# Performance work log

Measured on AMD Instinct MI355X. Metric: run time of the kernel, lower is better.

## Reference

```python
import jax, jax.numpy as jnp
import numpy as np


def setup_inputs() -> dict:
    key = jax.random.key(0)
    k1, k2 = jax.random.split(key)
    B, N, M, D = 4, 4096, 4096, 32
    x1 = jax.random.normal(k1, (B, N, D), dtype=jnp.float32)
    x2 = jax.random.normal(k2, (B, M, D), dtype=jnp.float32)
    const = jnp.ones((1,), dtype=jnp.float32)
    return {"x1": x1, "x2": x2, "const": const}


def reference(x1, x2, const):
    # Pairwise dot products: [B,N,D] x [B,M,D] -> [B,N,M], then add scalar bias.
    # (Original materializes an O(N*M*D) broadcast intermediate; einsum/bmm avoids it.)
    numerator = jnp.einsum("bnd,bmd->bnm", x1, x2)
    return numerator + const
```

## Files before the change

kernel.cpp:

```cpp
#include <hip/hip_runtime.h>


constexpr int Bv = 4;
constexpr int Nv = 4096;
constexpr int Mv = 4096;
constexpr int Dv = 32;
constexpr int TM = 128;
constexpr int TN = 256;
constexpr int LRA = 132;
constexpr int LRB = 260;

__global__ __launch_bounds__(256, 2)
void pairwise_dot_bias_kernel(const float* __restrict__ x1,
                              const float* __restrict__ x2,
                              const float* __restrict__ cbias,
                              float* __restrict__ out) {
    __shared__ float a_s[Dv][LRA];
    __shared__ float b_s[Dv][LRB];

    const int b  = blockIdx.z;
    const int n0 = blockIdx.y * TM;
    const int m0 = blockIdx.x * TN;
    const int t  = threadIdx.x;

    const float* x1b = x1 + (size_t)b * Nv * Dv + (size_t)n0 * Dv;
    const float* x2b = x2 + (size_t)b * Mv * Dv + (size_t)m0 * Dv;

    #pragma unroll
    for (int p = 0; p < 4; ++p) {
        const int flat = p * 1024 + t * 4;
        const int row  = flat >> 5;
        const int col  = flat & 31;
        const float4 av = *reinterpret_cast<const float4*>(x1b + flat);
        a_s[col + 0][row] = av.x;
        a_s[col + 1][row] = av.y;
        a_s[col + 2][row] = av.z;
        a_s[col + 3][row] = av.w;
    }
    #pragma unroll
    for (int p = 0; p < 8; ++p) {
        const int flat = p * 1024 + t * 4;
        const int row  = flat >> 5;
        const int col  = flat & 31;
        const float4 bv = *reinterpret_cast<const float4*>(x2b + flat);
        b_s[col + 0][row] = bv.x;
        b_s[col + 1][row] = bv.y;
        b_s[col + 2][row] = bv.z;
        b_s[col + 3][row] = bv.w;
    }
    __syncthreads();

    const int tx = t & 15;
    const int ty = t >> 4;

    float acc[8][16];
    #pragma unroll
    for (int i = 0; i < 8; ++i)
        #pragma unroll
        for (int j = 0; j < 16; ++j)
            acc[i][j] = 0.0f;

    #pragma unroll 2
    for (int d = 0; d < Dv; ++d) {
        const float4 a0 = *reinterpret_cast<const float4*>(&a_s[d][ty * 8]);
        const float4 a1 = *reinterpret_cast<const float4*>(&a_s[d][ty * 8 + 4]);
        const float4 b0 = *reinterpret_cast<const float4*>(&b_s[d][tx * 4]);
        const float4 b1 = *reinterpret_cast<const float4*>(&b_s[d][64 + tx * 4]);
        const float4 b2 = *reinterpret_cast<const float4*>(&b_s[d][128 + tx * 4]);
        const float4 b3 = *reinterpret_cast<const float4*>(&b_s[d][192 + tx * 4]);
        const float av[8]  = {a0.x, a0.y, a0.z, a0.w, a1.x, a1.y, a1.z, a1.w};
        const float bw[16] = {b0.x, b0.y, b0.z, b0.w, b1.x, b1.y, b1.z, b1.w,
                              b2.x, b2.y, b2.z, b2.w, b3.x, b3.y, b3.z, b3.w};
        #pragma unroll
        for (int i = 0; i < 8; ++i)
            #pragma unroll
            for (int j = 0; j < 16; ++j)
                acc[i][j] = fmaf(av[i], bw[j], acc[i][j]);
    }

    const float cb = cbias[0];
    float* outb = out + (size_t)b * Nv * Mv;
    #pragma unroll
    for (int i = 0; i < 8; ++i) {
        float* orow = outb + (size_t)(n0 + ty * 8 + i) * Mv + m0;
        #pragma unroll
        for (int h = 0; h < 4; ++h) {
            float4 v;
            v.x = acc[i][h * 4 + 0] + cb;
            v.y = acc[i][h * 4 + 1] + cb;
            v.z = acc[i][h * 4 + 2] + cb;
            v.w = acc[i][h * 4 + 3] + cb;
            *reinterpret_cast<float4*>(orow + h * 64 + tx * 4) = v;
        }
    }
}

extern "C" void kernel_launch(void* const* d_in, const int* in_sizes, int n_in,
                              void* d_out, int out_size, void* d_ws, size_t ws_size,
                              hipStream_t stream) {
    const float* x1 = (const float*)d_in[0];
    const float* x2 = (const float*)d_in[1];
    const float* cb = (const float*)d_in[2];
    float* out = (float*)d_out;

    dim3 grid(Mv / TN, Nv / TM, Bv);
    pairwise_dot_bias_kernel<<<grid, 256, 0, stream>>>(x1, x2, cb, out);
}
```

Before: 66.75 us.

## Loop each block over four N-tiles with double-buffered A prefetch and nontemporal stores

Each block now keeps its x2 tile resident in LDS and walks four consecutive 128-row x1 tiles. It prefetches the next x1 tile into registers while the current tile computes, and writes it into a second LDS buffer after the output stores. Output writes switch to nontemporal stores so they do not pollute the cache. This cuts the grid size and redundant B loads and overlaps global loads with compute, at the cost of more LDS, more registers for the prefetch, and less block-level parallelism.

```diff
diff --git a/kernel.cpp b/kernel.cpp
--- a/kernel.cpp
+++ b/kernel.cpp
@@ -1,5 +1,7 @@
 #include <hip/hip_runtime.h>
 
+
+typedef float v4f __attribute__((ext_vector_type(4)));
 
 constexpr int Bv = 4;
 constexpr int Nv = 4096;
@@ -7,6 +9,7 @@
 constexpr int Dv = 32;
 constexpr int TM = 128;
 constexpr int TN = 256;
+constexpr int NT = 4;
 constexpr int LRA = 132;
 constexpr int LRB = 260;
 
@@ -15,82 +18,114 @@
                               const float* __restrict__ x2,
                               const float* __restrict__ cbias,
                               float* __restrict__ out) {
-    __shared__ float a_s[Dv][LRA];
     __shared__ float b_s[Dv][LRB];
+    __shared__ float a_s[2][Dv][LRA];
 
-    const int b  = blockIdx.z;
-    const int n0 = blockIdx.y * TM;
-    const int m0 = blockIdx.x * TN;
-    const int t  = threadIdx.x;
+    const int b   = blockIdx.z;
+    const int m0  = blockIdx.x * TN;
+    const int n00 = blockIdx.y * (TM * NT);
+    const int t   = threadIdx.x;
 
-    const float* x1b = x1 + (size_t)b * Nv * Dv + (size_t)n0 * Dv;
     const float* x2b = x2 + (size_t)b * Mv * Dv + (size_t)m0 * Dv;
+    const float* x1b = x1 + (size_t)b * Nv * Dv + (size_t)n00 * Dv;
 
+    #pragma unroll
+    for (int p = 0; p < 8; ++p) {
+        const int flat = p * 1024 + t * 4;
+        const int row  = flat >> 5;
+        const int col  = flat & 31;
+        const v4f v = *reinterpret_cast<const v4f*>(x2b + flat);
+        b_s[col + 0][row] = v.x;
+        b_s[col + 1][row] = v.y;
+        b_s[col + 2][row] = v.z;
+        b_s[col + 3][row] = v.w;
+    }
     #pragma unroll
     for (int p = 0; p < 4; ++p) {
         const int flat = p * 1024 + t * 4;
         const int row  = flat >> 5;
         const int col  = flat & 31;
-        const float4 av = *reinterpret_cast<const float4*>(x1b + flat);
-        a_s[col + 0][row] = av.x;
-        a_s[col + 1][row] = av.y;
-        a_s[col + 2][row] = av.z;
-        a_s[col + 3][row] = av.w;
-    }
-    #pragma unroll
-    for (int p = 0; p < 8; ++p) {
-        const int flat = p * 1024 + t * 4;
-        const int row  = flat >> 5;
-        const int col  = flat & 31;
-        const float4 bv = *reinterpret_cast<const float4*>(x2b + flat);
-        b_s[col + 0][row] = bv.x;
-        b_s[col + 1][row] = bv.y;
-        b_s[col + 2][row] = bv.z;
-        b_s[col + 3][row] = bv.w;
+        const v4f v = *reinterpret_cast<const v4f*>(x1b + flat);
+        a_s[0][col + 0][row] = v.x;
+        a_s[0][col + 1][row] = v.y;
+        a_s[0][col + 2][row] = v.z;
+        a_s[0][col + 3][row] = v.w;
     }
     __syncthreads();
 
     const int tx = t & 15;
     const int ty = t >> 4;
+    const float cb = cbias[0];
+    float* outb = out + (size_t)b * Nv * Mv + m0;
 
-    float acc[8][16];
-    #pragma unroll
-    for (int i = 0; i < 8; ++i)
-        #pragma unroll
-        for (int j = 0; j < 16; ++j)
-            acc[i][j] = 0.0f;
+    for (int it = 0; it < NT; ++it) {
+        const int cur = it & 1;
 
-    #pragma unroll 2
-    for (int d = 0; d < Dv; ++d) {
-        const float4 a0 = *reinterpret_cast<const float4*>(&a_s[d][ty * 8]);
-        const float4 a1 = *reinterpret_cast<const float4*>(&a_s[d][ty * 8 + 4]);
-        const float4 b0 = *reinterpret_cast<const float4*>(&b_s[d][tx * 4]);
-        const float4 b1 = *reinterpret_cast<const float4*>(&b_s[d][64 + tx * 4]);
-        const float4 b2 = *reinterpret_cast<const float4*>(&b_s[d][128 + tx * 4]);
-        const float4 b3 = *reinterpret_cast<const float4*>(&b_s[d][192 + tx * 4]);
-        const float av[8]  = {a0.x, a0.y, a0.z, a0.w, a1.x, a1.y, a1.z, a1.w};
-        const float bw[16] = {b0.x, b0.y, b0.z, b0.w, b1.x, b1.y, b1.z, b1.w,
-                              b2.x, b2.y, b2.z, b2.w, b3.x, b3.y, b3.z, b3.w};
+        v4f pf[4];
+        if (it + 1 < NT) {
+            const float* src = x1b + (size_t)(it + 1) * TM * Dv;
+            #pragma unroll
+            for (int p = 0; p < 4; ++p)
+                pf[p] = *reinterpret_cast<const v4f*>(src + p * 1024 + t * 4);
+        }
+        asm volatile("" ::: "memory");
+
+        float acc[8][16];
         #pragma unroll
         for (int i = 0; i < 8; ++i)
             #pragma unroll
             for (int j = 0; j < 16; ++j)
-                acc[i][j] = fmaf(av[i], bw[j], acc[i][j]);
-    }
+                acc[i][j] = 0.0f;
 
-    const float cb = cbias[0];
-    float* outb = out + (size_t)b * Nv * Mv;
-    #pragma unroll
-    for (int i = 0; i < 8; ++i) {
-        float* orow = outb + (size_t)(n0 + ty * 8 + i) * Mv + m0;
+        #pragma unroll 2
+        for (int d = 0; d < Dv; ++d) {
+            const v4f a0 = *reinterpret_cast<const v4f*>(&a_s[cur][d][ty * 8]);
+            const v4f a1 = *reinterpret_cast<const v4f*>(&a_s[cur][d][ty * 8 + 4]);
+            const v4f b0 = *reinterpret_cast<const v4f*>(&b_s[d][tx * 4]);
+            const v4f b1 = *reinterpret_cast<const v4f*>(&b_s[d][64 + tx * 4]);
+            const v4f b2 = *reinterpret_cast<const v4f*>(&b_s[d][128 + tx * 4]);
+            const v4f b3 = *reinterpret_cast<const v4f*>(&b_s[d][192 + tx * 4]);
+            const float av[8]  = {a0.x, a0.y, a0.z, a0.w, a1.x, a1.y, a1.z, a1.w};
+            const float bw[16] = {b0.x, b0.y, b0.z, b0.w, b1.x, b1.y, b1.z, b1.w,
+                                  b2.x, b2.y, b2.z, b2.w, b3.x, b3.y, b3.z, b3.w};
+            #pragma unroll
+            for (int i = 0; i < 8; ++i)
+                #pragma unroll
+                for (int j = 0; j < 16; ++j)
+                    acc[i][j] = fmaf(av[i], bw[j], acc[i][j]);
+        }
+
+        const size_t rbase = (size_t)(n00 + it * TM + ty * 8);
         #pragma unroll
-        for (int h = 0; h < 4; ++h) {
-            float4 v;
-            v.x = acc[i][h * 4 + 0] + cb;
-            v.y = acc[i][h * 4 + 1] + cb;
-            v.z = acc[i][h * 4 + 2] + cb;
-            v.w = acc[i][h * 4 + 3] + cb;
-            *reinterpret_cast<float4*>(orow + h * 64 + tx * 4) = v;
+        for (int i = 0; i < 8; ++i) {
+            float* orow = outb + (rbase + i) * Mv;
+            #pragma unroll
+            for (int h = 0; h < 4; ++h) {
+                v4f v;
+                v.x = acc[i][h * 4 + 0] + cb;
+                v.y = acc[i][h * 4 + 1] + cb;
+                v.z = acc[i][h * 4 + 2] + cb;
+                v.w = acc[i][h * 4 + 3] + cb;
+                __builtin_nontemporal_store(
+                    v, reinterpret_cast<v4f*>(orow + h * 64 + tx * 4));
+            }
+        }
+        asm volatile("" ::: "memory");
+
+        if (it + 1 < NT) {
+            #pragma unroll
+            for (int p = 0; p < 4; ++p) {
+                const int flat = p * 1024 + t * 4;
+                const int row  = flat >> 5;
+                const int col  = flat & 31;
+                a_s[cur ^ 1][col + 0][row] = pf[p].x;
+                a_s[cur ^ 1][col + 1][row] = pf[p].y;
+                a_s[cur ^ 1][col + 2][row] = pf[p].z;
+                a_s[cur ^ 1][col + 3][row] = pf[p].w;
+            }
+            asm volatile("s_waitcnt lgkmcnt(0)" ::: "memory");
+            __builtin_amdgcn_s_barrier();
+            asm volatile("" ::: "memory");
         }
     }
 }
@@ -103,6 +138,6 @@
     const float* cb = (const float*)d_in[2];
     float* out = (float*)d_out;
 
-    dim3 grid(Mv / TN, Nv / TM, Bv);
+    dim3 grid(Mv / TN, Nv / (TM * NT), Bv);
     pairwise_dot_bias_kernel<<<grid, 256, 0, stream>>>(x1, x2, cb, out);
 }
```

Result: slower. 75.18 us (+12.6%).
